# Kernel optimization log

Measured on AMD Instinct MI355X. Metric: run time of the kernel, lower is better.

The kernel has to match this reference:

```python
import jax, jax.numpy as jnp
import numpy as np

B, S, D = 8, 2048, 512
LN_EPS = 1e-5

def _layernorm(x, gamma, beta):
    mu = jnp.mean(x, axis=-1, keepdims=True)
    var = jnp.mean(jnp.square(x - mu), axis=-1, keepdims=True)
    return (x - mu) * jax.lax.rsqrt(var + LN_EPS) * gamma + beta

def setup_inputs() -> dict:
    key = jax.random.key(0)
    ks = jax.random.split(key, 10)
    s_in = 1.0 / np.sqrt(2 * D)
    s_d = 1.0 / np.sqrt(D)
    return {
        "Noise_x": jax.random.normal(ks[0], (B, S, D), jnp.float32),
        "X": jax.random.normal(ks[1], (B, S, D), jnp.float32),
        "cond": jax.random.normal(ks[2], (B, S, D), jnp.float32),
        "W_gate": jax.random.normal(ks[3], (2 * D, D), jnp.float32) * s_in,
        "b_gate": jnp.zeros((D,), jnp.float32),
        "W1": jax.random.normal(ks[4], (D, 2 * D), jnp.float32) * s_d,
        "b1": jnp.zeros((2 * D,), jnp.float32),
        "W2": jax.random.normal(ks[5], (2 * D, D), jnp.float32) * s_in,
        "b2": jnp.zeros((D,), jnp.float32),
        "g1": jnp.ones((D,), jnp.float32),
        "be1": jnp.zeros((D,), jnp.float32),
        "g2": jnp.ones((D,), jnp.float32),
        "be2": jnp.zeros((D,), jnp.float32),
    }

def reference(Noise_x, X, cond, W_gate, b_gate, W1, b1, W2, b2, g1, be1, g2, be2):
    # gated fusion of noise and condition
    combined = jnp.concatenate([Noise_x, cond], axis=-1)            # [B,S,2D]
    gate = jax.nn.sigmoid(combined @ W_gate + b_gate)               # [B,S,D]
    fused = gate * Noise_x + (1.0 - gate) * cond                    # [B,S,D]
    # hand-rolled attention: Q = fused, K = V = X
    scale = 1.0 / jnp.sqrt(jnp.asarray(D, fused.dtype))
    scores = jnp.einsum('bqd,bkd->bqk', fused, X) * scale           # [B,S,S]
    attn = jax.nn.softmax(scores, axis=-1)
    attn_out = jnp.einsum('bqk,bkd->bqd', attn, X)                  # [B,S,D]
    # residual + norm, FFN (exact GELU as in torch default), residual + norm
    q = _layernorm(fused + attn_out, g1, be1)
    ff = jax.nn.gelu(q @ W1 + b1, approximate=False) @ W2 + b2
    return _layernorm(q + ff, g2, be2)
```

## Files before the change

### kernel.cpp

```cpp
#include <hip/hip_runtime.h>
#include <math.h>

typedef unsigned short ushort_t;
typedef unsigned int uint_t;
typedef __attribute__((ext_vector_type(8))) short short8;
typedef __attribute__((ext_vector_type(4))) float floatx4;

constexpr int B = 8;
constexpr int S = 2048;
constexpr int D = 512;
constexpr int BS = B * S;
constexpr float LN_EPS = 1e-5f;
constexpr float ATTN_SCALE = 0.04419417382415922f;


__device__ __forceinline__ ushort_t f2bf(float f) {
    union { float f; uint_t u; } x; x.f = f;
    uint_t r = x.u + 0x7fffu + ((x.u >> 16) & 1u);
    return (ushort_t)(r >> 16);
}
__device__ __forceinline__ float bf2f(ushort_t h) {
    union { uint_t u; float f; } y; y.u = ((uint_t)h) << 16;
    return y.f;
}
__device__ __forceinline__ short8 pack8(float4 a, float4 b) {
    short8 p;
    p[0] = (short)f2bf(a.x); p[1] = (short)f2bf(a.y);
    p[2] = (short)f2bf(a.z); p[3] = (short)f2bf(a.w);
    p[4] = (short)f2bf(b.x); p[5] = (short)f2bf(b.y);
    p[6] = (short)f2bf(b.z); p[7] = (short)f2bf(b.w);
    return p;
}

__device__ __forceinline__ float blk_reduce_sum(float v, float* sm) {
#pragma unroll
    for (int o = 32; o; o >>= 1) v += __shfl_down(v, o, 64);
    __syncthreads();
    if ((threadIdx.x & 63) == 0) sm[threadIdx.x >> 6] = v;
    __syncthreads();
    return sm[0] + sm[1] + sm[2] + sm[3];
}
__device__ __forceinline__ float blk_reduce_max(float v, float* sm) {
#pragma unroll
    for (int o = 32; o; o >>= 1) v = fmaxf(v, __shfl_down(v, o, 64));
    __syncthreads();
    if ((threadIdx.x & 63) == 0) sm[threadIdx.x >> 6] = v;
    __syncthreads();
    return fmaxf(fmaxf(sm[0], sm[1]), fmaxf(sm[2], sm[3]));
}

__global__ __launch_bounds__(256) void transpose_cvt(
    const float* __restrict__ in, ushort_t* __restrict__ out, int R, int C) {
    __shared__ float tl[32][33];
    const size_t zoff = (size_t)blockIdx.z * R * C;
    const int tx = threadIdx.x & 31, ty = threadIdx.x >> 5;
    const int c0 = blockIdx.x * 32, r0 = blockIdx.y * 32;
#pragma unroll
    for (int i = 0; i < 4; i++)
        tl[ty + i * 8][tx] = in[zoff + (size_t)(r0 + ty + i * 8) * C + c0 + tx];
    __syncthreads();
#pragma unroll
    for (int i = 0; i < 4; i++)
        out[zoff + (size_t)(c0 + ty + i * 8) * R + r0 + tx] = f2bf(tl[tx][ty + i * 8]);
}

#define GEMM_PREAMBLE()                                                        \
    __shared__ ushort_t As[128 * 40];                                          \
    __shared__ ushort_t Bs[128 * 40];                                          \
    const int t = threadIdx.x;                                                 \
    const int m0 = blockIdx.y * 128, n0 = blockIdx.x * 128;                    \
    const int sr = t >> 2;                                          \
    const int sc = (t & 3) * 8;                                 \
    const int lane = t & 63, w = t >> 6;                                       \
    const int wm = (w >> 1) * 64, wn = (w & 1) * 64;                           \
    const int fr = lane & 15, fq = lane >> 4;                                  \
    floatx4 acc[4][4];                                                         \
    _Pragma("unroll") for (int i = 0; i < 4; i++)                              \
        _Pragma("unroll") for (int j = 0; j < 4; j++) {                        \
            acc[i][j][0] = 0.f; acc[i][j][1] = 0.f;                            \
            acc[i][j][2] = 0.f; acc[i][j][3] = 0.f; }

#define GEMM_MFMA_STAGE()                                                      \
    short8 af[4], bfg[4];                                                      \
    _Pragma("unroll") for (int i = 0; i < 4; i++) {                            \
        af[i]  = *(const short8*)&As[(wm + i * 16 + fr) * 40 + fq * 8];        \
        bfg[i] = *(const short8*)&Bs[(wn + i * 16 + fr) * 40 + fq * 8];        \
    }                                                                          \
    _Pragma("unroll") for (int i = 0; i < 4; i++)                              \
        _Pragma("unroll") for (int j = 0; j < 4; j++)                          \
            acc[i][j] = __builtin_amdgcn_mfma_f32_16x16x32_bf16(               \
                af[i], bfg[j], acc[i][j], 0, 0, 0);

__global__ __launch_bounds__(256) void gate_gemm(
    const float* __restrict__ NX, const float* __restrict__ CD,
    const ushort_t* __restrict__ WgT, const float* __restrict__ bg,
    ushort_t* __restrict__ Fb) {
    GEMM_PREAMBLE();
    const ushort_t* Bb = WgT + (size_t)n0 * 1024;

    for (int k0 = 0; k0 < 1024; k0 += 32) {
        const float* Asrc = (k0 < 512) ? NX : CD;
        const int kk = k0 & 511;
        const float* p0 = Asrc + (size_t)(m0 + sr) * 512 + kk + sc;
        const float* p1 = Asrc + (size_t)(m0 + sr + 64) * 512 + kk + sc;
        float4 f00 = *(const float4*)p0;       float4 f01 = *(const float4*)(p0 + 4);
        float4 f10 = *(const float4*)p1;       float4 f11 = *(const float4*)(p1 + 4);
        int4 b0 = *(const int4*)(Bb + (size_t)sr * 1024 + k0 + sc);
        int4 b1 = *(const int4*)(Bb + (size_t)(sr + 64) * 1024 + k0 + sc);
        short8 pa0 = pack8(f00, f01), pa1 = pack8(f10, f11);
        __syncthreads();
        *(short8*)&As[sr * 40 + sc] = pa0;
        *(short8*)&As[(sr + 64) * 40 + sc] = pa1;
        *(int4*)&Bs[sr * 40 + sc] = b0;
        *(int4*)&Bs[(sr + 64) * 40 + sc] = b1;
        __syncthreads();
        GEMM_MFMA_STAGE();
    }

#pragma unroll
    for (int i = 0; i < 4; i++) {
#pragma unroll
        for (int j = 0; j < 4; j++) {
#pragma unroll
            for (int r = 0; r < 4; r++) {
                const int m = m0 + wm + i * 16 + fq * 4 + r;
                const int n = n0 + wn + j * 16 + fr;
                const float z = acc[i][j][r] + bg[n];
                const float g = 1.f / (1.f + expf(-z));
                const size_t idx = (size_t)m * 512 + n;
                Fb[idx] = f2bf(g * NX[idx] + (1.f - g) * CD[idx]);
            }
        }
    }
}

#define GEMM3_PREAMBLE()                                                       \
    __shared__ ushort_t As[128 * 40];                                          \
    __shared__ ushort_t Bs[64 * 40];                                           \
    const int t = threadIdx.x;                                                 \
    const int m0 = blockIdx.y * 128, n0 = blockIdx.x * 64;                     \
    const int sr = t >> 2;                                          \
    const int sc = (t & 3) * 8;                                 \
    const int lane = t & 63, w = t >> 6;                                       \
    const int wm = w * 32;                                                     \
    const int fr = lane & 15, fq = lane >> 4;                                  \
    floatx4 acc[2][4];                                                         \
    _Pragma("unroll") for (int i = 0; i < 2; i++)                              \
        _Pragma("unroll") for (int j = 0; j < 4; j++) {                        \
            acc[i][j][0] = 0.f; acc[i][j][1] = 0.f;                            \
            acc[i][j][2] = 0.f; acc[i][j][3] = 0.f; }

#define GEMM3_MFMA_STAGE()                                                     \
    short8 af[2], bfg[4];                                                      \
    _Pragma("unroll") for (int i = 0; i < 2; i++)                              \
        af[i]  = *(const short8*)&As[(wm + i * 16 + fr) * 40 + fq * 8];        \
    _Pragma("unroll") for (int j = 0; j < 4; j++)                              \
        bfg[j] = *(const short8*)&Bs[(j * 16 + fr) * 40 + fq * 8];             \
    _Pragma("unroll") for (int i = 0; i < 2; i++)                              \
        _Pragma("unroll") for (int j = 0; j < 4; j++)                          \
            acc[i][j] = __builtin_amdgcn_mfma_f32_16x16x32_bf16(               \
                af[i], bfg[j], acc[i][j], 0, 0, 0);

template <int EPI>
__global__ __launch_bounds__(256) void gemm3_std(
    const ushort_t* __restrict__ A, int lda, long sAz,
    const ushort_t* __restrict__ Bt, int ldb, long sBz,
    void* __restrict__ Cv, int ldc, long sCz,
    int K, const float* __restrict__ bias, float scale, int init) {
    GEMM3_PREAMBLE();
    const ushort_t* Ab = A + (size_t)blockIdx.z * sAz + (size_t)m0 * lda;
    const ushort_t* Bb = Bt + (size_t)blockIdx.z * sBz + (size_t)n0 * ldb;

    for (int k0 = 0; k0 < K; k0 += 32) {
        int4 a0 = *(const int4*)(Ab + (size_t)sr * lda + k0 + sc);
        int4 a1 = *(const int4*)(Ab + (size_t)(sr + 64) * lda + k0 + sc);
        int4 b0 = *(const int4*)(Bb + (size_t)sr * ldb + k0 + sc);
        __syncthreads();
        *(int4*)&As[sr * 40 + sc] = a0;
        *(int4*)&As[(sr + 64) * 40 + sc] = a1;
        *(int4*)&Bs[sr * 40 + sc] = b0;
        __syncthreads();
        GEMM3_MFMA_STAGE();
    }

#pragma unroll
    for (int i = 0; i < 2; i++) {
#pragma unroll
        for (int j = 0; j < 4; j++) {
#pragma unroll
            for (int r = 0; r < 4; r++) {
                const int m = m0 + wm + i * 16 + fq * 4 + r;
                const int n = n0 + j * 16 + fr;
                float v = acc[i][j][r];
                if (EPI == 0) {
                    ushort_t* C = (ushort_t*)Cv + (size_t)blockIdx.z * sCz;
                    C[(size_t)m * ldc + n] = f2bf(v * scale);
                } else if (EPI == 1) {
                    const float x = v + bias[n];
                    const float gl = 0.5f * x * (1.f + erff(x * 0.70710678118654752f));
                    ushort_t* C = (ushort_t*)Cv;
                    C[(size_t)m * ldc + n] = f2bf(gl);
                } else {
                    float* T = (float*)Cv;
                    const size_t idx = (size_t)m * ldc + n;
                    T[idx] = T[idx] + v + (init ? bias[n] : 0.f);
                }
            }
        }
    }
}

__global__ __launch_bounds__(256) void qk_gemm3(
    const ushort_t* __restrict__ Qb, const float* __restrict__ Xf,
    ushort_t* __restrict__ Sc) {
    GEMM3_PREAMBLE();
    const ushort_t* Ab = Qb + (size_t)blockIdx.z * S * D + (size_t)m0 * D;
    const float*    Bf = Xf + (size_t)blockIdx.z * S * D + (size_t)n0 * D;
    ushort_t* Scb = Sc + (size_t)blockIdx.z * S * S;

    for (int k0 = 0; k0 < D; k0 += 32) {
        int4 a0 = *(const int4*)(Ab + (size_t)sr * D + k0 + sc);
        int4 a1 = *(const int4*)(Ab + (size_t)(sr + 64) * D + k0 + sc);
        const float* p0 = Bf + (size_t)sr * D + k0 + sc;
        float4 f00 = *(const float4*)p0;       float4 f01 = *(const float4*)(p0 + 4);
        short8 pb0 = pack8(f00, f01);
        __syncthreads();
        *(int4*)&As[sr * 40 + sc] = a0;
        *(int4*)&As[(sr + 64) * 40 + sc] = a1;
        *(short8*)&Bs[sr * 40 + sc] = pb0;
        __syncthreads();
        GEMM3_MFMA_STAGE();
    }

#pragma unroll
    for (int i = 0; i < 2; i++) {
#pragma unroll
        for (int j = 0; j < 4; j++) {
#pragma unroll
            for (int r = 0; r < 4; r++) {
                const int m = m0 + wm + i * 16 + fq * 4 + r;
                const int n = n0 + j * 16 + fr;
                Scb[(size_t)m * S + n] = f2bf(acc[i][j][r] * ATTN_SCALE);
            }
        }
    }
}

__global__ __launch_bounds__(256) void softmax_bf16(ushort_t* __restrict__ Sc) {
    __shared__ float sm[4];
    ushort_t* row = Sc + (size_t)blockIdx.x * 2048;
    const int t = threadIdx.x;
    ushort_t raw[8];
    *(int4*)raw = *(const int4*)(row + t * 8);
    float e[8];
    float mx = -1e30f;
#pragma unroll
    for (int j = 0; j < 8; j++) { e[j] = bf2f(raw[j]); mx = fmaxf(mx, e[j]); }
    mx = blk_reduce_max(mx, sm);
    float s = 0.f;
#pragma unroll
    for (int j = 0; j < 8; j++) { e[j] = expf(e[j] - mx); s += e[j]; }
    s = blk_reduce_sum(s, sm);
    const float inv = 1.f / s;
#pragma unroll
    for (int j = 0; j < 8; j++) raw[j] = f2bf(e[j] * inv);
    *(int4*)(row + t * 8) = *(const int4*)raw;
}

__global__ __launch_bounds__(256) void ln1_kernel(
    const ushort_t* __restrict__ Fb, const ushort_t* __restrict__ Ab,
    const float* __restrict__ g1, const float* __restrict__ be1,
    float* __restrict__ qf, ushort_t* __restrict__ qb) {
    __shared__ float sm[4];
    const size_t base = (size_t)blockIdx.x * 512;
    const int t = threadIdx.x;
    const float v0 = bf2f(Fb[base + t]) + bf2f(Ab[base + t]);
    const float v1 = bf2f(Fb[base + t + 256]) + bf2f(Ab[base + t + 256]);
    const float mu = blk_reduce_sum(v0 + v1, sm) * (1.f / 512.f);
    const float d0 = v0 - mu, d1 = v1 - mu;
    const float var = blk_reduce_sum(d0 * d0 + d1 * d1, sm) * (1.f / 512.f);
    const float rs = rsqrtf(var + LN_EPS);
    const float y0 = d0 * rs * g1[t] + be1[t];
    const float y1 = d1 * rs * g1[t + 256] + be1[t + 256];
    qf[base + t] = y0;          qf[base + t + 256] = y1;
    qb[base + t] = f2bf(y0);    qb[base + t + 256] = f2bf(y1);
}

__global__ __launch_bounds__(256) void ln2_kernel(
    float* __restrict__ T, const float* __restrict__ g,
    const float* __restrict__ be) {
    __shared__ float sm[4];
    const size_t base = (size_t)blockIdx.x * 512;
    const int t = threadIdx.x;
    const float v0 = T[base + t];
    const float v1 = T[base + t + 256];
    const float mu = blk_reduce_sum(v0 + v1, sm) * (1.f / 512.f);
    const float d0 = v0 - mu, d1 = v1 - mu;
    const float var = blk_reduce_sum(d0 * d0 + d1 * d1, sm) * (1.f / 512.f);
    const float rs = rsqrtf(var + LN_EPS);
    T[base + t] = d0 * rs * g[t] + be[t];
    T[base + t + 256] = d1 * rs * g[t + 256] + be[t + 256];
}

extern "C" void kernel_launch(void* const* d_in, const int* in_sizes, int n_in,
                              void* d_out, int out_size, void* d_ws, size_t ws_size,
                              hipStream_t stream) {
    const float* NX  = (const float*)d_in[0];
    const float* X   = (const float*)d_in[1];
    const float* CD  = (const float*)d_in[2];
    const float* Wg  = (const float*)d_in[3];
    const float* bg  = (const float*)d_in[4];
    const float* W1  = (const float*)d_in[5];
    const float* b1  = (const float*)d_in[6];
    const float* W2  = (const float*)d_in[7];
    const float* b2  = (const float*)d_in[8];
    const float* g1  = (const float*)d_in[9];
    const float* be1 = (const float*)d_in[10];
    const float* g2  = (const float*)d_in[11];
    const float* be2 = (const float*)d_in[12];

    ushort_t* slot0 = (ushort_t*)d_ws;
    ushort_t* slot1 = (ushort_t*)((char*)d_ws + 16777216);
    ushort_t* slot2 = (ushort_t*)((char*)d_ws + 33554432);
    ushort_t* attnb = slot0;
    ushort_t* hbuf  = slot0;
    ushort_t* Fb    = slot1;
    ushort_t* W1T   = slot1;
    ushort_t* W2T   = slot1 + 524288;
    ushort_t* WgT   = slot2;
    ushort_t* XbT   = slot2;
    ushort_t* qb    = slot2;
    ushort_t* Scb   = (ushort_t*)d_out;
    float*    qf    = (float*)d_out;

    transpose_cvt<<<dim3(512 / 32, 1024 / 32, 1), 256, 0, stream>>>(Wg, WgT, 1024, 512);

    gate_gemm<<<dim3(4, 128), 256, 0, stream>>>(NX, CD, WgT, bg, Fb);

    transpose_cvt<<<dim3(512 / 32, 2048 / 32, 8), 256, 0, stream>>>(X, XbT, 2048, 512);

    for (int g = 0; g < 2; g++) {
        const size_t go = (size_t)g * 4 * S * 512;
        qk_gemm3<<<dim3(32, 16, 4), 256, 0, stream>>>(Fb + go, X + go, Scb);
        softmax_bf16<<<4 * S, 256, 0, stream>>>(Scb);
        gemm3_std<0><<<dim3(8, 16, 4), 256, 0, stream>>>(
            Scb, S, (long)S * S,
            XbT + go, S, (long)D * S,
            (void*)(attnb + go), 512, (long)S * 512, S, nullptr, 1.f, 0);
    }

    ln1_kernel<<<BS, 256, 0, stream>>>(Fb, attnb, g1, be1, qf, qb);

    transpose_cvt<<<dim3(1024 / 32, 512 / 32, 1), 256, 0, stream>>>(W1, W1T, 512, 1024);
    transpose_cvt<<<dim3(512 / 32, 1024 / 32, 1), 256, 0, stream>>>(W2, W2T, 1024, 512);

    for (int h = 0; h < 2; h++) {
        gemm3_std<1><<<dim3(8, 128), 256, 0, stream>>>(
            qb, 512, 0, W1T + (size_t)h * 512 * 512, 512, 0,
            (void*)hbuf, 512, 0, 512, b1 + h * 512, 1.f, 0);
        gemm3_std<2><<<dim3(8, 128), 256, 0, stream>>>(
            hbuf, 512, 0, W2T + h * 512, 1024, 0,
            (void*)qf, 512, 0, 512, b2, 1.f, h == 0 ? 1 : 0);
    }

    ln2_kernel<<<BS, 256, 0, stream>>>(qf, g2, be2);
}
```

Before: 555.3 us.

## Enlarge GEMM tiles to 128x128x64 and pre-convert X to bf16 for QK

```diff
diff --git a/kernel.cpp b/kernel.cpp
--- a/kernel.cpp
+++ b/kernel.cpp
@@ -50,14 +50,18 @@
 }
 
 __global__ __launch_bounds__(256) void transpose_cvt(
-    const float* __restrict__ in, ushort_t* __restrict__ out, int R, int C) {
+    const float* __restrict__ in, ushort_t* __restrict__ out, int R, int C,
+    ushort_t* __restrict__ out2) {
     __shared__ float tl[32][33];
     const size_t zoff = (size_t)blockIdx.z * R * C;
     const int tx = threadIdx.x & 31, ty = threadIdx.x >> 5;
     const int c0 = blockIdx.x * 32, r0 = blockIdx.y * 32;
 #pragma unroll
-    for (int i = 0; i < 4; i++)
-        tl[ty + i * 8][tx] = in[zoff + (size_t)(r0 + ty + i * 8) * C + c0 + tx];
+    for (int i = 0; i < 4; i++) {
+        const float v = in[zoff + (size_t)(r0 + ty + i * 8) * C + c0 + tx];
+        tl[ty + i * 8][tx] = v;
+        if (out2) out2[zoff + (size_t)(r0 + ty + i * 8) * C + c0 + tx] = f2bf(v);
+    }
     __syncthreads();
 #pragma unroll
     for (int i = 0; i < 4; i++)
@@ -134,63 +138,70 @@
     }
 }
 
-#define GEMM3_PREAMBLE()                                                       \
-    __shared__ ushort_t As[128 * 40];                                          \
-    __shared__ ushort_t Bs[64 * 40];                                           \
+#define GEMM4_PREAMBLE()                                                       \
+    __shared__ ushort_t As[128 * 72];                                          \
+    __shared__ ushort_t Bs[128 * 72];                                          \
     const int t = threadIdx.x;                                                 \
-    const int m0 = blockIdx.y * 128, n0 = blockIdx.x * 64;                     \
-    const int sr = t >> 2;                                          \
-    const int sc = (t & 3) * 8;                                 \
+    const int m0 = blockIdx.y * 128, n0 = blockIdx.x * 128;                    \
+    const int sr8 = t >> 3;                                         \
+    const int sc8 = (t & 7) * 8;                             \
     const int lane = t & 63, w = t >> 6;                                       \
-    const int wm = w * 32;                                                     \
+    const int wm = (w >> 1) * 64, wn = (w & 1) * 64;                           \
     const int fr = lane & 15, fq = lane >> 4;                                  \
-    floatx4 acc[2][4];                                                         \
-    _Pragma("unroll") for (int i = 0; i < 2; i++)                              \
+    floatx4 acc[4][4];                                                         \
+    _Pragma("unroll") for (int i = 0; i < 4; i++)                              \
         _Pragma("unroll") for (int j = 0; j < 4; j++) {                        \
             acc[i][j][0] = 0.f; acc[i][j][1] = 0.f;                            \
             acc[i][j][2] = 0.f; acc[i][j][3] = 0.f; }
 
-#define GEMM3_MFMA_STAGE()                                                     \
-    short8 af[2], bfg[4];                                                      \
-    _Pragma("unroll") for (int i = 0; i < 2; i++)                              \
-        af[i]  = *(const short8*)&As[(wm + i * 16 + fr) * 40 + fq * 8];        \
-    _Pragma("unroll") for (int j = 0; j < 4; j++)                              \
-        bfg[j] = *(const short8*)&Bs[(j * 16 + fr) * 40 + fq * 8];             \
-    _Pragma("unroll") for (int i = 0; i < 2; i++)                              \
-        _Pragma("unroll") for (int j = 0; j < 4; j++)                          \
-            acc[i][j] = __builtin_amdgcn_mfma_f32_16x16x32_bf16(               \
-                af[i], bfg[j], acc[i][j], 0, 0, 0);
+#define GEMM4_K_STEP(Ab, lda, Bb, ldb, k0)                                     \
+    {                                                                          \
+        int4 ra[4], rb[4];                                                     \
+        _Pragma("unroll") for (int i = 0; i < 4; i++) {                        \
+            ra[i] = *(const int4*)(Ab + (size_t)(sr8 + i * 32) * lda + k0 + sc8); \
+            rb[i] = *(const int4*)(Bb + (size_t)(sr8 + i * 32) * ldb + k0 + sc8); \
+        }                                                                      \
+        __syncthreads();                                                       \
+        _Pragma("unroll") for (int i = 0; i < 4; i++) {                        \
+            *(int4*)&As[(sr8 + i * 32) * 72 + sc8] = ra[i];                    \
+            *(int4*)&Bs[(sr8 + i * 32) * 72 + sc8] = rb[i];                    \
+        }                                                                      \
+        __syncthreads();                                                       \
+        _Pragma("unroll") for (int kk = 0; kk < 2; kk++) {                     \
+            short8 af[4], bfg[4];                                              \
+            _Pragma("unroll") for (int i = 0; i < 4; i++) {                    \
+                af[i]  = *(const short8*)&As[(wm + i * 16 + fr) * 72 + kk * 32 + fq * 8]; \
+                bfg[i] = *(const short8*)&Bs[(wn + i * 16 + fr) * 72 + kk * 32 + fq * 8]; \
+            }                                                                  \
+            _Pragma("unroll") for (int i = 0; i < 4; i++)                      \
+                _Pragma("unroll") for (int j = 0; j < 4; j++)                  \
+                    acc[i][j] = __builtin_amdgcn_mfma_f32_16x16x32_bf16(       \
+                        af[i], bfg[j], acc[i][j], 0, 0, 0);                    \
+        }                                                                      \
+    }
 
 template <int EPI>
-__global__ __launch_bounds__(256) void gemm3_std(
+__global__ __launch_bounds__(256) void gemm4_std(
     const ushort_t* __restrict__ A, int lda, long sAz,
     const ushort_t* __restrict__ Bt, int ldb, long sBz,
     void* __restrict__ Cv, int ldc, long sCz,
     int K, const float* __restrict__ bias, float scale, int init) {
-    GEMM3_PREAMBLE();
+    GEMM4_PREAMBLE();
     const ushort_t* Ab = A + (size_t)blockIdx.z * sAz + (size_t)m0 * lda;
     const ushort_t* Bb = Bt + (size_t)blockIdx.z * sBz + (size_t)n0 * ldb;
 
-    for (int k0 = 0; k0 < K; k0 += 32) {
-        int4 a0 = *(const int4*)(Ab + (size_t)sr * lda + k0 + sc);
-        int4 a1 = *(const int4*)(Ab + (size_t)(sr + 64) * lda + k0 + sc);
-        int4 b0 = *(const int4*)(Bb + (size_t)sr * ldb + k0 + sc);
-        __syncthreads();
-        *(int4*)&As[sr * 40 + sc] = a0;
-        *(int4*)&As[(sr + 64) * 40 + sc] = a1;
-        *(int4*)&Bs[sr * 40 + sc] = b0;
-        __syncthreads();
-        GEMM3_MFMA_STAGE();
-    }
-
-#pragma unroll
-    for (int i = 0; i < 2; i++) {
+    for (int k0 = 0; k0 < K; k0 += 64) {
+        GEMM4_K_STEP(Ab, lda, Bb, ldb, k0);
+    }
+
+#pragma unroll
+    for (int i = 0; i < 4; i++) {
 #pragma unroll
         for (int j = 0; j < 4; j++) {
 #pragma unroll
             for (int r = 0; r < 4; r++) {
                 const int m = m0 + wm + i * 16 + fq * 4 + r;
-                const int n = n0 + j * 16 + fr;
+                const int n = n0 + wn + j * 16 + fr;
                 float v = acc[i][j][r];
                 if (EPI == 0) {
                     ushort_t* C = (ushort_t*)Cv + (size_t)blockIdx.z * sCz;
@@ -205,42 +216,6 @@
                     const size_t idx = (size_t)m * ldc + n;
                     T[idx] = T[idx] + v + (init ? bias[n] : 0.f);
                 }
-            }
-        }
-    }
-}
-
-__global__ __launch_bounds__(256) void qk_gemm3(
-    const ushort_t* __restrict__ Qb, const float* __restrict__ Xf,
-    ushort_t* __restrict__ Sc) {
-    GEMM3_PREAMBLE();
-    const ushort_t* Ab = Qb + (size_t)blockIdx.z * S * D + (size_t)m0 * D;
-    const float*    Bf = Xf + (size_t)blockIdx.z * S * D + (size_t)n0 * D;
-    ushort_t* Scb = Sc + (size_t)blockIdx.z * S * S;
-
-    for (int k0 = 0; k0 < D; k0 += 32) {
-        int4 a0 = *(const int4*)(Ab + (size_t)sr * D + k0 + sc);
-        int4 a1 = *(const int4*)(Ab + (size_t)(sr + 64) * D + k0 + sc);
-        const float* p0 = Bf + (size_t)sr * D + k0 + sc;
-        float4 f00 = *(const float4*)p0;       float4 f01 = *(const float4*)(p0 + 4);
-        short8 pb0 = pack8(f00, f01);
-        __syncthreads();
-        *(int4*)&As[sr * 40 + sc] = a0;
-        *(int4*)&As[(sr + 64) * 40 + sc] = a1;
-        *(short8*)&Bs[sr * 40 + sc] = pb0;
-        __syncthreads();
-        GEMM3_MFMA_STAGE();
-    }
-
-#pragma unroll
-    for (int i = 0; i < 2; i++) {
-#pragma unroll
-        for (int j = 0; j < 4; j++) {
-#pragma unroll
-            for (int r = 0; r < 4; r++) {
-                const int m = m0 + wm + i * 16 + fq * 4 + r;
-                const int n = n0 + j * 16 + fr;
-                Scb[(size_t)m * S + n] = f2bf(acc[i][j][r] * ATTN_SCALE);
             }
         }
     }
@@ -322,6 +297,7 @@
     ushort_t* slot0 = (ushort_t*)d_ws;
     ushort_t* slot1 = (ushort_t*)((char*)d_ws + 16777216);
     ushort_t* slot2 = (ushort_t*)((char*)d_ws + 33554432);
+    ushort_t* Xb    = slot0;
     ushort_t* attnb = slot0;
     ushort_t* hbuf  = slot0;
     ushort_t* Fb    = slot1;
@@ -333,17 +309,22 @@
     ushort_t* Scb   = (ushort_t*)d_out;
     float*    qf    = (float*)d_out;
 
-    transpose_cvt<<<dim3(512 / 32, 1024 / 32, 1), 256, 0, stream>>>(Wg, WgT, 1024, 512);
+    transpose_cvt<<<dim3(512 / 32, 1024 / 32, 1), 256, 0, stream>>>(
+        Wg, WgT, 1024, 512, nullptr);
 
     gate_gemm<<<dim3(4, 128), 256, 0, stream>>>(NX, CD, WgT, bg, Fb);
 
-    transpose_cvt<<<dim3(512 / 32, 2048 / 32, 8), 256, 0, stream>>>(X, XbT, 2048, 512);
+    transpose_cvt<<<dim3(512 / 32, 2048 / 32, 8), 256, 0, stream>>>(
+        X, XbT, 2048, 512, Xb);
 
     for (int g = 0; g < 2; g++) {
         const size_t go = (size_t)g * 4 * S * 512;
-        qk_gemm3<<<dim3(32, 16, 4), 256, 0, stream>>>(Fb + go, X + go, Scb);
+        gemm4_std<0><<<dim3(16, 16, 4), 256, 0, stream>>>(
+            Fb + go, D, (long)S * D,
+            Xb + go, D, (long)S * D,
+            (void*)Scb, S, (long)S * S, D, nullptr, ATTN_SCALE, 0);
         softmax_bf16<<<4 * S, 256, 0, stream>>>(Scb);
-        gemm3_std<0><<<dim3(8, 16, 4), 256, 0, stream>>>(
+        gemm4_std<0><<<dim3(4, 16, 4), 256, 0, stream>>>(
             Scb, S, (long)S * S,
             XbT + go, S, (long)D * S,
             (void*)(attnb + go), 512, (long)S * 512, S, nullptr, 1.f, 0);
@@ -351,14 +332,16 @@
 
     ln1_kernel<<<BS, 256, 0, stream>>>(Fb, attnb, g1, be1, qf, qb);
 
-    transpose_cvt<<<dim3(1024 / 32, 512 / 32, 1), 256, 0, stream>>>(W1, W1T, 512, 1024);
-    transpose_cvt<<<dim3(512 / 32, 1024 / 32, 1), 256, 0, stream>>>(W2, W2T, 1024, 512);
+    transpose_cvt<<<dim3(1024 / 32, 512 / 32, 1), 256, 0, stream>>>(
+        W1, W1T, 512, 1024, nullptr);
+    transpose_cvt<<<dim3(512 / 32, 1024 / 32, 1), 256, 0, stream>>>(
+        W2, W2T, 1024, 512, nullptr);
 
     for (int h = 0; h < 2; h++) {
-        gemm3_std<1><<<dim3(8, 128), 256, 0, stream>>>(
+        gemm4_std<1><<<dim3(4, 128), 256, 0, stream>>>(
             qb, 512, 0, W1T + (size_t)h * 512 * 512, 512, 0,
             (void*)hbuf, 512, 0, 512, b1 + h * 512, 1.f, 0);
-        gemm3_std<2><<<dim3(8, 128), 256, 0, stream>>>(
+        gemm4_std<2><<<dim3(4, 128), 256, 0, stream>>>(
             hbuf, 512, 0, W2T + h * 512, 1024, 0,
             (void*)qf, 512, 0, 512, b2, 1.f, h == 0 ? 1 : 0);
     }
```

Result: slower. 848.2 us (+52.8%).

## Prefetch next K-tile into registers in GEMMs and precompute bf16 X for QK

Applied to the files above, without the earlier changes.

```diff
diff --git a/kernel.cpp b/kernel.cpp
--- a/kernel.cpp
+++ b/kernel.cpp
@@ -50,14 +50,18 @@
 }
 
 __global__ __launch_bounds__(256) void transpose_cvt(
-    const float* __restrict__ in, ushort_t* __restrict__ out, int R, int C) {
+    const float* __restrict__ in, ushort_t* __restrict__ out, int R, int C,
+    ushort_t* __restrict__ out2) {
     __shared__ float tl[32][33];
     const size_t zoff = (size_t)blockIdx.z * R * C;
     const int tx = threadIdx.x & 31, ty = threadIdx.x >> 5;
     const int c0 = blockIdx.x * 32, r0 = blockIdx.y * 32;
 #pragma unroll
-    for (int i = 0; i < 4; i++)
-        tl[ty + i * 8][tx] = in[zoff + (size_t)(r0 + ty + i * 8) * C + c0 + tx];
+    for (int i = 0; i < 4; i++) {
+        const float v = in[zoff + (size_t)(r0 + ty + i * 8) * C + c0 + tx];
+        tl[ty + i * 8][tx] = v;
+        if (out2) out2[zoff + (size_t)(r0 + ty + i * 8) * C + c0 + tx] = f2bf(v);
+    }
     __syncthreads();
 #pragma unroll
     for (int i = 0; i < 4; i++)
@@ -98,22 +102,36 @@
     GEMM_PREAMBLE();
     const ushort_t* Bb = WgT + (size_t)n0 * 1024;
 
+    float4 f00, f01, f10, f11;
+    int4 b0, b1;
+    {
+        const float* p0 = NX + (size_t)(m0 + sr) * 512 + sc;
+        const float* p1 = NX + (size_t)(m0 + sr + 64) * 512 + sc;
+        f00 = *(const float4*)p0;  f01 = *(const float4*)(p0 + 4);
+        f10 = *(const float4*)p1;  f11 = *(const float4*)(p1 + 4);
+        b0 = *(const int4*)(Bb + (size_t)sr * 1024 + sc);
+        b1 = *(const int4*)(Bb + (size_t)(sr + 64) * 1024 + sc);
+    }
+
     for (int k0 = 0; k0 < 1024; k0 += 32) {
-        const float* Asrc = (k0 < 512) ? NX : CD;
-        const int kk = k0 & 511;
-        const float* p0 = Asrc + (size_t)(m0 + sr) * 512 + kk + sc;
-        const float* p1 = Asrc + (size_t)(m0 + sr + 64) * 512 + kk + sc;
-        float4 f00 = *(const float4*)p0;       float4 f01 = *(const float4*)(p0 + 4);
-        float4 f10 = *(const float4*)p1;       float4 f11 = *(const float4*)(p1 + 4);
-        int4 b0 = *(const int4*)(Bb + (size_t)sr * 1024 + k0 + sc);
-        int4 b1 = *(const int4*)(Bb + (size_t)(sr + 64) * 1024 + k0 + sc);
+        __syncthreads();
         short8 pa0 = pack8(f00, f01), pa1 = pack8(f10, f11);
-        __syncthreads();
         *(short8*)&As[sr * 40 + sc] = pa0;
         *(short8*)&As[(sr + 64) * 40 + sc] = pa1;
         *(int4*)&Bs[sr * 40 + sc] = b0;
         *(int4*)&Bs[(sr + 64) * 40 + sc] = b1;
         __syncthreads();
+        const int kn = k0 + 32;
+        if (kn < 1024) {
+            const float* Asrc = (kn < 512) ? NX : CD;
+            const int kk = kn & 511;
+            const float* p0 = Asrc + (size_t)(m0 + sr) * 512 + kk + sc;
+            const float* p1 = Asrc + (size_t)(m0 + sr + 64) * 512 + kk + sc;
+            f00 = *(const float4*)p0;  f01 = *(const float4*)(p0 + 4);
+            f10 = *(const float4*)p1;  f11 = *(const float4*)(p1 + 4);
+            b0 = *(const int4*)(Bb + (size_t)sr * 1024 + kn + sc);
+            b1 = *(const int4*)(Bb + (size_t)(sr + 64) * 1024 + kn + sc);
+        }
         GEMM_MFMA_STAGE();
     }
 
@@ -171,15 +189,22 @@
     const ushort_t* Ab = A + (size_t)blockIdx.z * sAz + (size_t)m0 * lda;
     const ushort_t* Bb = Bt + (size_t)blockIdx.z * sBz + (size_t)n0 * ldb;
 
+    int4 a0 = *(const int4*)(Ab + (size_t)sr * lda + sc);
+    int4 a1 = *(const int4*)(Ab + (size_t)(sr + 64) * lda + sc);
+    int4 b0 = *(const int4*)(Bb + (size_t)sr * ldb + sc);
+
     for (int k0 = 0; k0 < K; k0 += 32) {
-        int4 a0 = *(const int4*)(Ab + (size_t)sr * lda + k0 + sc);
-        int4 a1 = *(const int4*)(Ab + (size_t)(sr + 64) * lda + k0 + sc);
-        int4 b0 = *(const int4*)(Bb + (size_t)sr * ldb + k0 + sc);
         __syncthreads();
         *(int4*)&As[sr * 40 + sc] = a0;
         *(int4*)&As[(sr + 64) * 40 + sc] = a1;
         *(int4*)&Bs[sr * 40 + sc] = b0;
         __syncthreads();
+        const int kn = k0 + 32;
+        if (kn < K) {
+            a0 = *(const int4*)(Ab + (size_t)sr * lda + kn + sc);
+            a1 = *(const int4*)(Ab + (size_t)(sr + 64) * lda + kn + sc);
+            b0 = *(const int4*)(Bb + (size_t)sr * ldb + kn + sc);
+        }
         GEMM3_MFMA_STAGE();
     }
 
@@ -210,42 +235,6 @@
     }
 }
 
-__global__ __launch_bounds__(256) void qk_gemm3(
-    const ushort_t* __restrict__ Qb, const float* __restrict__ Xf,
-    ushort_t* __restrict__ Sc) {
-    GEMM3_PREAMBLE();
-    const ushort_t* Ab = Qb + (size_t)blockIdx.z * S * D + (size_t)m0 * D;
-    const float*    Bf = Xf + (size_t)blockIdx.z * S * D + (size_t)n0 * D;
-    ushort_t* Scb = Sc + (size_t)blockIdx.z * S * S;
-
-    for (int k0 = 0; k0 < D; k0 += 32) {
-        int4 a0 = *(const int4*)(Ab + (size_t)sr * D + k0 + sc);
-        int4 a1 = *(const int4*)(Ab + (size_t)(sr + 64) * D + k0 + sc);
-        const float* p0 = Bf + (size_t)sr * D + k0 + sc;
-        float4 f00 = *(const float4*)p0;       float4 f01 = *(const float4*)(p0 + 4);
-        short8 pb0 = pack8(f00, f01);
-        __syncthreads();
-        *(int4*)&As[sr * 40 + sc] = a0;
-        *(int4*)&As[(sr + 64) * 40 + sc] = a1;
-        *(short8*)&Bs[sr * 40 + sc] = pb0;
-        __syncthreads();
-        GEMM3_MFMA_STAGE();
-    }
-
-#pragma unroll
-    for (int i = 0; i < 2; i++) {
-#pragma unroll
-        for (int j = 0; j < 4; j++) {
-#pragma unroll
-            for (int r = 0; r < 4; r++) {
-                const int m = m0 + wm + i * 16 + fq * 4 + r;
-                const int n = n0 + j * 16 + fr;
-                Scb[(size_t)m * S + n] = f2bf(acc[i][j][r] * ATTN_SCALE);
-            }
-        }
-    }
-}
-
 __global__ __launch_bounds__(256) void softmax_bf16(ushort_t* __restrict__ Sc) {
     __shared__ float sm[4];
     ushort_t* row = Sc + (size_t)blockIdx.x * 2048;
@@ -322,6 +311,7 @@
     ushort_t* slot0 = (ushort_t*)d_ws;
     ushort_t* slot1 = (ushort_t*)((char*)d_ws + 16777216);
     ushort_t* slot2 = (ushort_t*)((char*)d_ws + 33554432);
+    ushort_t* Xb    = slot0;
     ushort_t* attnb = slot0;
     ushort_t* hbuf  = slot0;
     ushort_t* Fb    = slot1;
@@ -333,15 +323,20 @@
     ushort_t* Scb   = (ushort_t*)d_out;
     float*    qf    = (float*)d_out;
 
-    transpose_cvt<<<dim3(512 / 32, 1024 / 32, 1), 256, 0, stream>>>(Wg, WgT, 1024, 512);
+    transpose_cvt<<<dim3(512 / 32, 1024 / 32, 1), 256, 0, stream>>>(
+        Wg, WgT, 1024, 512, nullptr);
 
     gate_gemm<<<dim3(4, 128), 256, 0, stream>>>(NX, CD, WgT, bg, Fb);
 
-    transpose_cvt<<<dim3(512 / 32, 2048 / 32, 8), 256, 0, stream>>>(X, XbT, 2048, 512);
+    transpose_cvt<<<dim3(512 / 32, 2048 / 32, 8), 256, 0, stream>>>(
+        X, XbT, 2048, 512, Xb);
 
     for (int g = 0; g < 2; g++) {
         const size_t go = (size_t)g * 4 * S * 512;
-        qk_gemm3<<<dim3(32, 16, 4), 256, 0, stream>>>(Fb + go, X + go, Scb);
+        gemm3_std<0><<<dim3(32, 16, 4), 256, 0, stream>>>(
+            Fb + go, D, (long)S * D,
+            Xb + go, D, (long)S * D,
+            (void*)Scb, S, (long)S * S, D, nullptr, ATTN_SCALE, 0);
         softmax_bf16<<<4 * S, 256, 0, stream>>>(Scb);
         gemm3_std<0><<<dim3(8, 16, 4), 256, 0, stream>>>(
             Scb, S, (long)S * S,
@@ -351,8 +346,10 @@
 
     ln1_kernel<<<BS, 256, 0, stream>>>(Fb, attnb, g1, be1, qf, qb);
 
-    transpose_cvt<<<dim3(1024 / 32, 512 / 32, 1), 256, 0, stream>>>(W1, W1T, 512, 1024);
-    transpose_cvt<<<dim3(512 / 32, 1024 / 32, 1), 256, 0, stream>>>(W2, W2T, 1024, 512);
+    transpose_cvt<<<dim3(1024 / 32, 512 / 32, 1), 256, 0, stream>>>(
+        W1, W1T, 512, 1024, nullptr);
+    transpose_cvt<<<dim3(512 / 32, 1024 / 32, 1), 256, 0, stream>>>(
+        W2, W2T, 1024, 512, nullptr);
 
     for (int h = 0; h < 2; h++) {
         gemm3_std<1><<<dim3(8, 128), 256, 0, stream>>>(
```

Measured after the change: 545.3 us. About the same (-1.8%).
